# Kernel optimization log

Measured on AMD Instinct MI355X. Metric: run time of the kernel, lower is better.

## Reference

```python
import jax, jax.numpy as jnp
import numpy as np

NUM_VERTS = 6890
NUM_JOINTS = 24
NUM_BETAS = 10
NUM_POSE_FEATS = 207  # 23 joints * 9
NUM_COCO_JOINTS = 19
BATCH = 1024

SMPL_PARENTS = np.array([0, 0, 0, 0, 1, 2, 3, 4, 5, 6, 7, 8, 9, 9, 9,
                         12, 13, 14, 16, 17, 18, 19, 20, 21], dtype=np.int32)


def batch_rodrigues(theta):
    """theta: [N,3] axis-angle -> [N,3,3] rotation matrices (Rodrigues)."""
    angle = jnp.linalg.norm(theta + 1e-8, axis=1, keepdims=True)  # [N,1]
    r = theta / angle                                             # [N,3]
    c = jnp.cos(angle)[:, :, None]                                # [N,1,1]
    s = jnp.sin(angle)[:, :, None]
    rx, ry, rz = r[:, 0], r[:, 1], r[:, 2]
    zeros = jnp.zeros_like(rx)
    K = jnp.stack([zeros, -rz, ry,
                   rz, zeros, -rx,
                   -ry, rx, zeros], axis=1).reshape(-1, 3, 3)     # skew(r)
    eye = jnp.eye(3, dtype=theta.dtype)
    return eye + s * K + (1.0 - c) * jnp.matmul(K, K)


def batch_global_rigid_transformation(Rs, Js, parents, rotate_base=True):
    """Rs: [B,24,3,3], Js: [B,24,3]. Returns (new_J [B,24,3], A [B,24,4,4])."""
    B = Rs.shape[0]
    dtype = Rs.dtype
    if rotate_base:
        rot_x = jnp.array([[1., 0., 0.], [0., -1., 0.], [0., 0., -1.]], dtype=dtype)
        root_rot = jnp.matmul(Rs[:, 0], rot_x)
    else:
        root_rot = Rs[:, 0]

    bottom = jnp.broadcast_to(jnp.array([0., 0., 0., 1.], dtype=dtype), (B, 1, 4))

    def make_A(R, t):  # R [B,3,3], t [B,3] -> [B,4,4]
        top = jnp.concatenate([R, t[:, :, None]], axis=2)  # [B,3,4]
        return jnp.concatenate([top, bottom], axis=1)

    results = [make_A(root_rot, Js[:, 0])]
    for i in range(1, NUM_JOINTS):
        t_rel = Js[:, i] - Js[:, parents[i]]
        A_here = make_A(Rs[:, i], t_rel)
        results.append(jnp.matmul(results[parents[i]], A_here))
    results = jnp.stack(results, axis=1)  # [B,24,4,4]

    new_J = results[:, :, :3, 3]
    # A = results - pad(results @ [J;0]) : subtract rotated rest joint from translation
    t_adj = jnp.einsum('bjpq,bjq->bjp', results[:, :, :3, :3], Js)  # [B,24,3]
    A = results.at[:, :, :3, 3].add(-t_adj)
    return new_J, A


def setup_inputs() -> dict:
    key = jax.random.key(0)
    ks = jax.random.split(key, 8)
    beta = jax.random.normal(ks[0], (BATCH, NUM_BETAS), dtype=jnp.float32)
    theta = jax.random.normal(ks[1], (BATCH, NUM_JOINTS * 3), dtype=jnp.float32) * 0.3
    v_template = jax.random.normal(ks[2], (NUM_VERTS, 3), dtype=jnp.float32)
    shapedirs = jax.random.normal(ks[3], (NUM_BETAS, NUM_VERTS * 3), dtype=jnp.float32) * 0.01
    J_regressor = jax.random.uniform(ks[4], (NUM_JOINTS, NUM_VERTS), dtype=jnp.float32) / NUM_VERTS
    posedirs = jax.random.normal(ks[5], (NUM_POSE_FEATS, NUM_VERTS * 3), dtype=jnp.float32) * 0.01
    joint_regressor = jax.random.uniform(ks[6], (NUM_COCO_JOINTS, NUM_VERTS), dtype=jnp.float32) / NUM_VERTS
    w_raw = jax.random.uniform(ks[7], (NUM_VERTS, NUM_JOINTS), dtype=jnp.float32)
    weights = w_raw / jnp.sum(w_raw, axis=1, keepdims=True)  # LBS weights, rows sum to 1
    parents = jnp.asarray(SMPL_PARENTS)
    return {"beta": beta, "theta": theta, "v_template": v_template,
            "shapedirs": shapedirs, "J_regressor": J_regressor,
            "posedirs": posedirs, "joint_regressor": joint_regressor,
            "weights": weights, "parents": parents}


def reference(beta, theta, v_template, shapedirs, J_regressor,
              posedirs, joint_regressor, weights, parents):
    B = beta.shape[0]
    parents_np = np.asarray(parents)

    # Shape blendshapes: [B,10]@[10,20670] -> [B,6890,3]
    v_shaped = jnp.matmul(beta, shapedirs).reshape(B, NUM_VERTS, 3) + v_template

    J = jnp.einsum('bvd,jv->bjd', v_shaped, J_regressor)

    # Pose rotations
    Rs = batch_rodrigues(theta.reshape(-1, 3)).reshape(B, NUM_JOINTS, 3, 3)
    pose_feature = (Rs[:, 1:] - jnp.eye(3, dtype=Rs.dtype)).reshape(B, NUM_POSE_FEATS)
    v_posed = jnp.matmul(pose_feature, posedirs).reshape(B, NUM_VERTS, 3) + v_shaped

    # Kinematic chain
    J_transformed, A = batch_global_rigid_transformation(Rs, J, parents_np, rotate_base=True)

    # Linear blend skinning: per-vertex 4x4 transforms
    T = jnp.einsum('vj,bjpq->bvpq', weights, A)  # [B,6890,4,4]
    ones = jnp.ones((B, NUM_VERTS, 1), dtype=v_posed.dtype)
    v_posed_homo = jnp.concatenate([v_posed, ones], axis=2)  # [B,6890,4]
    verts = jnp.einsum('bvpq,bvq->bvp', T[:, :, :3, :], v_posed_homo)  # [B,6890,3]

    joints = jnp.einsum('bvd,jv->bjd', verts, joint_regressor)  # [B,19,3]
    return verts, joints, Rs
```

## Files before the change

### kernel.cpp

```cpp
#include <hip/hip_runtime.h>
#include <math.h>

#define NV   6890
#define NJ   24
#define NB   10
#define NPF  207
#define NCJ  19
#define BATCHN 1024
#define NC3  (NV*3)
#define KTOT 224
#define NVP  6892

#define OUT_JOINTS_OFF (BATCHN*NV*3)
#define OUT_RS_OFF     (OUT_JOINTS_OFF + BATCHN*NCJ*3)

#define WS_JS     0
#define WS_EF     1024
#define WS_AADJT  115712
#define WS_JRB    377856
#define WS_DIRST  443392
#define WS_END    2765824

typedef __attribute__((ext_vector_type(8))) short short8;
typedef __attribute__((ext_vector_type(4))) float f32x4;

__device__ __forceinline__ unsigned short f2bf(float f) {
    unsigned u = __float_as_uint(f);
    unsigned r = u + 0x7FFFu + ((u >> 16) & 1u);
    return (unsigned short)(r >> 16);
}
__device__ __forceinline__ float bf2f(unsigned short u) {
    return __uint_as_float((unsigned)u << 16);
}

__global__ __launch_bounds__(256) void smpl_kAP(
    const float* __restrict__ pdirs, const float* __restrict__ sdirs,
    unsigned short* __restrict__ dirsT,
    const float* __restrict__ jreg, const float* __restrict__ vtmpl,
    float* __restrict__ js,
    const float* __restrict__ jointreg, unsigned short* __restrict__ jrb) {
    int bx = blockIdx.x, t = threadIdx.x;
    if (bx < 216) {
        int vt = bx;
        for (int g = t; g < 2688; g += 256) {
            int frag = g >> 6, fo = g & 63;
            int ks = frag / 6, s = frag - ks * 6;
            int l15 = fo >> 2, lg = fo & 3;
            int gc = vt * 96 + s * 16 + l15;
            int k0 = ks * 32 + lg * 8;
            unsigned short pk[8];
#pragma unroll
            for (int i = 0; i < 8; i++) {
                int k = k0 + i;
                float val = 0.f;
                if (gc < NC3) {
                    if (k < NPF) val = pdirs[(size_t)k * NC3 + gc];
                    else if (k < NPF + NB) val = sdirs[(size_t)(k - NPF) * NC3 + gc];
                }
                pk[i] = f2bf(val);
            }
            *(short8*)(dirsT + (size_t)vt * 21504 + (size_t)g * 8) = *(const short8*)pk;
        }
        return;
    }
    if (bx >= 216 + NJ) {
        int j = bx - 216 - NJ;
        for (int v = t; v < NVP; v += 256)
            jrb[(size_t)j * NVP + v] = (v < NV) ? f2bf(jointreg[(size_t)j * NV + v]) : 0;
        return;
    }
    int j = bx - 216;
    float acc[33];
#pragma unroll
    for (int e = 0; e < 33; e++) acc[e] = 0.f;
    for (int v = t; v < NV; v += 256) {
        float w = jreg[j * NV + v];
#pragma unroll
        for (int k = 0; k < NB; k++) {
#pragma unroll
            for (int d = 0; d < 3; d++)
                acc[k * 3 + d] += w * sdirs[(size_t)k * NC3 + v * 3 + d];
        }
#pragma unroll
        for (int d = 0; d < 3; d++) acc[30 + d] += w * vtmpl[v * 3 + d];
    }
#pragma unroll
    for (int e = 0; e < 33; e++) {
#pragma unroll
        for (int off = 32; off >= 1; off >>= 1) acc[e] += __shfl_xor(acc[e], off, 64);
    }
    __shared__ float red[4][33];
    int lane = t & 63, wv = t >> 6;
    if (lane == 0) {
#pragma unroll
        for (int e = 0; e < 33; e++) red[wv][e] = acc[e];
    }
    __syncthreads();
    if (t < 33) js[j * 33 + t] = red[0][t] + red[1][t] + red[2][t] + red[3][t];
}

__global__ void smpl_kB(const float* __restrict__ theta, const float* __restrict__ beta_,
                        const float* __restrict__ js, float* __restrict__ outRs,
                        unsigned short* __restrict__ ef, unsigned short* __restrict__ aadjT,
                        float* __restrict__ outj) {
    int b = blockIdx.x;
    int t = threadIdx.x;
    __shared__ float Rl[NJ][9];
    __shared__ float Jl[NJ][3];
    __shared__ float Rw[NJ][12];

    if (t < 57) outj[(size_t)b * 57 + t] = 0.f;

    if (t < NJ) {
        int j = t;
        float tx = theta[b * 72 + j * 3 + 0];
        float ty = theta[b * 72 + j * 3 + 1];
        float tz = theta[b * 72 + j * 3 + 2];
        float ax = tx + 1e-8f, ay = ty + 1e-8f, az = tz + 1e-8f;
        float ang = sqrtf(ax * ax + ay * ay + az * az);
        float inv = 1.0f / ang;
        float rx = tx * inv, ry = ty * inv, rz = tz * inv;
        float s = sinf(ang), c = cosf(ang), t1 = 1.0f - c;
        float R[9];
        R[0] = 1.0f - t1 * (ry * ry + rz * rz);
        R[1] = -s * rz + t1 * rx * ry;
        R[2] =  s * ry + t1 * rx * rz;
        R[3] =  s * rz + t1 * rx * ry;
        R[4] = 1.0f - t1 * (rx * rx + rz * rz);
        R[5] = -s * rx + t1 * ry * rz;
        R[6] = -s * ry + t1 * rx * rz;
        R[7] =  s * rx + t1 * ry * rz;
        R[8] = 1.0f - t1 * (rx * rx + ry * ry);
#pragma unroll
        for (int e = 0; e < 9; e++) {
            Rl[j][e] = R[e];
            outRs[(size_t)b * 216 + j * 9 + e] = R[e];
        }
#pragma unroll
        for (int d = 0; d < 3; d++) {
            float accJ = js[j * 33 + 30 + d];
#pragma unroll
            for (int k = 0; k < NB; k++) accJ += beta_[b * NB + k] * js[j * 33 + k * 3 + d];
            Jl[j][d] = accJ;
        }
    }
    __syncthreads();
    for (int e = t; e < KTOT; e += 64) {
        float val;
        if (e < NPF) {
            int j = e / 9 + 1;
            int rc = e - (j - 1) * 9;
            val = Rl[j][rc] - ((rc == 0 || rc == 4 || rc == 8) ? 1.0f : 0.0f);
        } else if (e < NPF + NB) {
            val = beta_[b * NB + (e - NPF)];
        } else val = 0.f;
        ef[(size_t)b * KTOT + e] = f2bf(val);
    }
    if (t == 0) {
#pragma unroll
        for (int r = 0; r < 3; r++) {
            Rw[0][r * 4 + 0] =  Rl[0][r * 3 + 0];
            Rw[0][r * 4 + 1] = -Rl[0][r * 3 + 1];
            Rw[0][r * 4 + 2] = -Rl[0][r * 3 + 2];
            Rw[0][r * 4 + 3] =  Jl[0][r];
        }
        const int par[NJ] = {0,0,0,0,1,2,3,4,5,6,7,8,9,9,9,12,13,14,16,17,18,19,20,21};
#pragma unroll
        for (int i = 1; i < NJ; i++) {
            int p = par[i];
            float tr0 = Jl[i][0] - Jl[p][0];
            float tr1 = Jl[i][1] - Jl[p][1];
            float tr2 = Jl[i][2] - Jl[p][2];
#pragma unroll
            for (int r = 0; r < 3; r++) {
                float p0 = Rw[p][r * 4 + 0], p1 = Rw[p][r * 4 + 1], p2 = Rw[p][r * 4 + 2];
#pragma unroll
                for (int cc = 0; cc < 3; cc++)
                    Rw[i][r * 4 + cc] = p0 * Rl[i][0 + cc] + p1 * Rl[i][3 + cc] + p2 * Rl[i][6 + cc];
                Rw[i][r * 4 + 3] = p0 * tr0 + p1 * tr1 + p2 * tr2 + Rw[p][r * 4 + 3];
            }
        }
    }
    __syncthreads();
    for (int i = t; i < 512; i += 64) {
        int n = i >> 5, k = i & 31;
        float v = 0.f;
        if (n < 12 && k < 24) {
            int r = n >> 2, cc = n & 3;
            if (cc < 3) v = Rw[k][n];
            else v = Rw[k][r * 4 + 3] - (Rw[k][r * 4 + 0] * Jl[k][0] + Rw[k][r * 4 + 1] * Jl[k][1] +
                                         Rw[k][r * 4 + 2] * Jl[k][2]);
        }
        aadjT[(size_t)b * 512 + i] = f2bf(v);
    }
}

#define VPHI(v, bl, d) (((v) * 133 + (bl)) * 4 + (d))
__global__ __launch_bounds__(512, 4) void smpl_kC7(
    const unsigned short* __restrict__ dirsT, const float* __restrict__ vtmpl,
    const unsigned short* __restrict__ ef, const unsigned short* __restrict__ aadjT,
    const float* __restrict__ wts, float* __restrict__ outv) {
    __shared__ __align__(16) unsigned short dl[21504];
    __shared__ __align__(16) unsigned short vph[32 * 133 * 4];
    __shared__ unsigned short wbf[32][32];

    int tid = threadIdx.x;
    int vtile = blockIdx.x;
    int lane = tid & 63, wv = tid >> 6;
    int l15 = lane & 15, lg = lane >> 4;
    int fo = l15 * 4 + lg;

    {
        const uint2* src = (const uint2*)(dirsT + (size_t)vtile * 21504);
        uint2* dst = (uint2*)dl;
        for (int i = tid; i < 5376; i += 512) dst[i] = src[i];
    }
    for (int e = tid; e < 1024; e += 512) {
        int vl = e >> 5, k = e & 31;
        int gv = vtile * 32 + vl;
        float w = (k < NJ && gv < NV) ? wts[(size_t)gv * NJ + k] : 0.f;
        wbf[vl][k] = f2bf(w);
    }
    __syncthreads();

    short8 wf0 = *(const short8*)&wbf[l15][lg * 8];
    short8 wf1 = *(const short8*)&wbf[16 + l15][lg * 8];
    float vt[6];
#pragma unroll
    for (int s = 0; s < 6; s++) {
        int gcol = vtile * 96 + s * 16 + l15;
        vt[s] = (gcol < NC3) ? vtmpl[gcol] : 0.f;
    }

    for (int bt = 0; bt < 2; bt++) {
        int bb = (blockIdx.y * 2 + bt) * 128 + wv * 16;
        const short8* efr = (const short8*)(ef + (size_t)(bb + l15) * KTOT);
        short8 av[7];
#pragma unroll
        for (int ks = 0; ks < 7; ks++) av[ks] = efr[ks * 4 + lg];
        const short8* at0 = (const short8*)(aadjT + (size_t)bb * 512);
        short8 af0 = at0[fo];
        short8 af1 = at0[64 + fo];
        __builtin_amdgcn_sched_barrier(0);

        f32x4 acc[6];
#pragma unroll
        for (int s = 0; s < 6; s++) acc[s] = (f32x4){0.f, 0.f, 0.f, 0.f};
#pragma unroll
        for (int ks = 0; ks < 7; ks++) {
#pragma unroll
            for (int s = 0; s < 6; s++) {
                short8 bv = *(const short8*)&dl[((ks * 6 + s) << 9) + fo * 8];
                acc[s] = __builtin_amdgcn_mfma_f32_16x16x32_bf16(av[ks], bv, acc[s], 0, 0, 0);
            }
        }
#pragma unroll
        for (int s = 0; s < 6; s++) {
            int col = s * 16 + l15;
            int v = col / 3, d = col - v * 3;
            int bl0 = wv * 16 + lg * 4;
#pragma unroll
            for (int r = 0; r < 4; r++)
                vph[VPHI(v, bl0 + r, d)] = f2bf(acc[s][r] + vt[s]);
        }
#pragma unroll
        for (int bl2 = 0; bl2 < 16; bl2++) {
            short8 af = af0;
            af0 = af1;
            int nx = (bl2 + 2 < 16) ? (bl2 + 2) : 15;
            af1 = at0[nx * 64 + fo];
            f32x4 z = (f32x4){0.f, 0.f, 0.f, 0.f};
            f32x4 t0 = __builtin_amdgcn_mfma_f32_16x16x32_bf16(af, wf0, z, 0, 0, 0);
            f32x4 t1 = __builtin_amdgcn_mfma_f32_16x16x32_bf16(af, wf1, z, 0, 0, 0);
            int b = bb + bl2;
            int wvb = wv * 16 + bl2;
            if (lg < 3) {
                int p = lg;
                {
                    int vv = l15;
                    ushort4 xv = *(const ushort4*)&vph[VPHI(vv, wvb, 0)];
                    float o = fmaf(t0[0], bf2f(xv.x),
                              fmaf(t0[1], bf2f(xv.y), fmaf(t0[2], bf2f(xv.z), t0[3])));
                    int gv = vtile * 32 + vv;
                    if (gv < NV) outv[(size_t)b * NC3 + gv * 3 + p] = o;
                }
                {
                    int vv = 16 + l15;
                    ushort4 xv = *(const ushort4*)&vph[VPHI(vv, wvb, 0)];
                    float o = fmaf(t1[0], bf2f(xv.x),
                              fmaf(t1[1], bf2f(xv.y), fmaf(t1[2], bf2f(xv.z), t1[3])));
                    int gv = vtile * 32 + vv;
                    if (gv < NV) outv[(size_t)b * NC3 + gv * 3 + p] = o;
                }
            }
        }
    }
}

__global__ __launch_bounds__(256) void smpl_kD(
    const float* __restrict__ verts, const unsigned short* __restrict__ jrb,
    float* __restrict__ outj) {
    int tid = threadIdx.x;
    int b = blockIdx.x >> 1, half = blockIdx.x & 1;
    const float* vb = verts + (size_t)b * NC3;
    float acc[57];
#pragma unroll
    for (int e = 0; e < 57; e++) acc[e] = 0.f;

    int gend = half ? 1723 : 862;
    for (int it = 0; it < 4; it++) {
        int g = half * 862 + it * 256 + tid;
        if (g < gend) {
            int v = g * 4;
            const float* pa = vb + v * 3;
            float2 q0 = *(const float2*)(pa + 0);
            float2 q1 = *(const float2*)(pa + 2);
            float2 q2 = *(const float2*)(pa + 4);
            float2 q3 = *(const float2*)(pa + 6);
            float2 q4 = *(const float2*)(pa + 8);
            float2 q5 = *(const float2*)(pa + 10);
#pragma unroll
            for (int j = 0; j < NCJ; j++) {
                uint2 wp = *(const uint2*)(jrb + (size_t)j * NVP + v);
                float w0 = __uint_as_float((wp.x & 0xFFFFu) << 16);
                float w1 = __uint_as_float(wp.x & 0xFFFF0000u);
                float w2 = __uint_as_float((wp.y & 0xFFFFu) << 16);
                float w3 = __uint_as_float(wp.y & 0xFFFF0000u);
                acc[j * 3 + 0] += w0 * q0.x + w1 * q1.y + w2 * q3.x + w3 * q4.y;
                acc[j * 3 + 1] += w0 * q0.y + w1 * q2.x + w2 * q3.y + w3 * q5.x;
                acc[j * 3 + 2] += w0 * q1.x + w1 * q2.y + w2 * q4.x + w3 * q5.y;
            }
        }
    }
#pragma unroll
    for (int e = 0; e < 57; e++) {
#pragma unroll
        for (int off = 32; off >= 1; off >>= 1) acc[e] += __shfl_xor(acc[e], off, 64);
    }
    __shared__ float red[4][57];
    int lane = tid & 63, wv = tid >> 6;
    if (lane == 0) {
#pragma unroll
        for (int e = 0; e < 57; e++) red[wv][e] = acc[e];
    }
    __syncthreads();
    if (tid < 57)
        atomicAdd(&outj[(size_t)b * 57 + tid],
                  red[0][tid] + red[1][tid] + red[2][tid] + red[3][tid]);
}

extern "C" void kernel_launch(void* const* d_in, const int* in_sizes, int n_in,
                              void* d_out, int out_size, void* d_ws, size_t ws_size,
                              hipStream_t stream) {
    (void)in_sizes; (void)n_in; (void)out_size; (void)ws_size;
    const float* beta       = (const float*)d_in[0];
    const float* theta      = (const float*)d_in[1];
    const float* v_template = (const float*)d_in[2];
    const float* shapedirs  = (const float*)d_in[3];
    const float* jreg       = (const float*)d_in[4];
    const float* posedirs   = (const float*)d_in[5];
    const float* jointreg   = (const float*)d_in[6];
    const float* weights    = (const float*)d_in[7];
    float* out = (float*)d_out;
    float* ws  = (float*)d_ws;
    unsigned short* ef    = (unsigned short*)(ws + WS_EF);
    unsigned short* aadjT = (unsigned short*)(ws + WS_AADJT);
    unsigned short* jrb   = (unsigned short*)(ws + WS_JRB);
    unsigned short* dirsT = (unsigned short*)(ws + WS_DIRST);

    smpl_kAP<<<216 + NJ + NCJ, 256, 0, stream>>>(posedirs, shapedirs, dirsT,
                                                 jreg, v_template, ws + WS_JS,
                                                 jointreg, jrb);
    smpl_kB<<<BATCHN, 64, 0, stream>>>(theta, beta, ws + WS_JS, out + OUT_RS_OFF,
                                       ef, aadjT, out + OUT_JOINTS_OFF);
    dim3 gC(216, 4);
    smpl_kC7<<<gC, 512, 0, stream>>>(dirsT, v_template, ef, aadjT, weights, out);
    smpl_kD<<<2 * BATCHN, 256, 0, stream>>>(out, jrb, out + OUT_JOINTS_OFF);
}
```

Before: 127.6 us.

## Batch-prefetch skinning transforms in chunks and process four batch tiles per block

In the skinning kernel, each block now loops over four 128-sample batch tiles instead of two, and the grid's y dimension is halved. This amortises the per-block staging of directions and weights into shared memory over more work. The per-sample transform loads are restructured from a rolling two-deep prefetch into two chunks of eight register-held loads, with the first chunk issued during the blendshape MFMA phase. Empty asm barriers pin the loads in place. The costs are higher register pressure and only 432 blocks, which may reduce occupancy and load balance.

```diff
diff --git a/kernel.cpp b/kernel.cpp
--- a/kernel.cpp
+++ b/kernel.cpp
@@ -232,16 +232,14 @@
         vt[s] = (gcol < NC3) ? vtmpl[gcol] : 0.f;
     }
 
-    for (int bt = 0; bt < 2; bt++) {
-        int bb = (blockIdx.y * 2 + bt) * 128 + wv * 16;
+    for (int bt = 0; bt < 4; bt++) {
+        int bb = (blockIdx.y * 4 + bt) * 128 + wv * 16;
         const short8* efr = (const short8*)(ef + (size_t)(bb + l15) * KTOT);
         short8 av[7];
 #pragma unroll
         for (int ks = 0; ks < 7; ks++) av[ks] = efr[ks * 4 + lg];
-        const short8* at0 = (const short8*)(aadjT + (size_t)bb * 512);
-        short8 af0 = at0[fo];
-        short8 af1 = at0[64 + fo];
-        __builtin_amdgcn_sched_barrier(0);
+#pragma unroll
+        for (int ks = 0; ks < 7; ks++) asm volatile("" : "+v"(av[ks]));
 
         f32x4 acc[6];
 #pragma unroll
@@ -254,6 +252,11 @@
                 acc[s] = __builtin_amdgcn_mfma_f32_16x16x32_bf16(av[ks], bv, acc[s], 0, 0, 0);
             }
         }
+        const short8* at0 = (const short8*)(aadjT + (size_t)bb * 512);
+        short8 afc[8];
+#pragma unroll
+        for (int i = 0; i < 8; i++) afc[i] = at0[i * 64 + fo];
+
 #pragma unroll
         for (int s = 0; s < 6; s++) {
             int col = s * 16 + l15;
@@ -264,33 +267,46 @@
                 vph[VPHI(v, bl0 + r, d)] = f2bf(acc[s][r] + vt[s]);
         }
 #pragma unroll
-        for (int bl2 = 0; bl2 < 16; bl2++) {
-            short8 af = af0;
-            af0 = af1;
-            int nx = (bl2 + 2 < 16) ? (bl2 + 2) : 15;
-            af1 = at0[nx * 64 + fo];
-            f32x4 z = (f32x4){0.f, 0.f, 0.f, 0.f};
-            f32x4 t0 = __builtin_amdgcn_mfma_f32_16x16x32_bf16(af, wf0, z, 0, 0, 0);
-            f32x4 t1 = __builtin_amdgcn_mfma_f32_16x16x32_bf16(af, wf1, z, 0, 0, 0);
-            int b = bb + bl2;
-            int wvb = wv * 16 + bl2;
-            if (lg < 3) {
-                int p = lg;
-                {
-                    int vv = l15;
-                    ushort4 xv = *(const ushort4*)&vph[VPHI(vv, wvb, 0)];
-                    float o = fmaf(t0[0], bf2f(xv.x),
-                              fmaf(t0[1], bf2f(xv.y), fmaf(t0[2], bf2f(xv.z), t0[3])));
-                    int gv = vtile * 32 + vv;
-                    if (gv < NV) outv[(size_t)b * NC3 + gv * 3 + p] = o;
-                }
-                {
-                    int vv = 16 + l15;
-                    ushort4 xv = *(const ushort4*)&vph[VPHI(vv, wvb, 0)];
-                    float o = fmaf(t1[0], bf2f(xv.x),
-                              fmaf(t1[1], bf2f(xv.y), fmaf(t1[2], bf2f(xv.z), t1[3])));
-                    int gv = vtile * 32 + vv;
-                    if (gv < NV) outv[(size_t)b * NC3 + gv * 3 + p] = o;
+        for (int i = 0; i < 8; i++) asm volatile("" : "+v"(afc[i]));
+        short8 afn[8];
+#pragma unroll
+        for (int i = 0; i < 8; i++) afn[i] = at0[(8 + i) * 64 + fo];
+
+#pragma unroll
+        for (int ch = 0; ch < 2; ch++) {
+            if (ch == 1) {
+#pragma unroll
+                for (int i = 0; i < 8; i++) asm volatile("" : "+v"(afn[i]));
+#pragma unroll
+                for (int i = 0; i < 8; i++) afc[i] = afn[i];
+            }
+#pragma unroll
+            for (int i = 0; i < 8; i++) {
+                short8 af = afc[i];
+                f32x4 z = (f32x4){0.f, 0.f, 0.f, 0.f};
+                f32x4 t0 = __builtin_amdgcn_mfma_f32_16x16x32_bf16(af, wf0, z, 0, 0, 0);
+                f32x4 t1 = __builtin_amdgcn_mfma_f32_16x16x32_bf16(af, wf1, z, 0, 0, 0);
+                int bl2 = ch * 8 + i;
+                int b = bb + bl2;
+                int wvb = wv * 16 + bl2;
+                if (lg < 3) {
+                    int p = lg;
+                    {
+                        int vv = l15;
+                        ushort4 xv = *(const ushort4*)&vph[VPHI(vv, wvb, 0)];
+                        float o = fmaf(t0[0], bf2f(xv.x),
+                                  fmaf(t0[1], bf2f(xv.y), fmaf(t0[2], bf2f(xv.z), t0[3])));
+                        int gv = vtile * 32 + vv;
+                        if (gv < NV) outv[(size_t)b * NC3 + gv * 3 + p] = o;
+                    }
+                    {
+                        int vv = 16 + l15;
+                        ushort4 xv = *(const ushort4*)&vph[VPHI(vv, wvb, 0)];
+                        float o = fmaf(t1[0], bf2f(xv.x),
+                                  fmaf(t1[1], bf2f(xv.y), fmaf(t1[2], bf2f(xv.z), t1[3])));
+                        int gv = vtile * 32 + vv;
+                        if (gv < NV) outv[(size_t)b * NC3 + gv * 3 + p] = o;
+                    }
                 }
             }
         }
@@ -373,7 +389,7 @@
                                                  jointreg, jrb);
     smpl_kB<<<BATCHN, 64, 0, stream>>>(theta, beta, ws + WS_JS, out + OUT_RS_OFF,
                                        ef, aadjT, out + OUT_JOINTS_OFF);
-    dim3 gC(216, 4);
+    dim3 gC(216, 2);
     smpl_kC7<<<gC, 512, 0, stream>>>(dirsT, v_template, ef, aadjT, weights, out);
     smpl_kD<<<2 * BATCHN, 256, 0, stream>>>(out, jrb, out + OUT_JOINTS_OFF);
 }
```

Measured after the change: 127.3 us. Within noise of the previous version (-0.2%).

## Drop LDS staging of blend-shape dirs in skinning kernel, use smaller blocks

Applied to the files above, without the earlier changes.

The skinning kernel no longer stages the 43KB bf16 direction tile in shared memory. Each wave now reads its B fragments straight from global memory, and blocks shrink to 256 threads covering 64 batch rows on a 216x16 grid. This cuts LDS use so more blocks can be resident per CU, at the cost of the same dirs tile being re-read from global/L2 by every block. The prep kernel's dirs-transpose stage is also split across six times as many blocks to expose more parallelism.

```diff
diff --git a/kernel.cpp b/kernel.cpp
--- a/kernel.cpp
+++ b/kernel.cpp
@@ -40,9 +40,9 @@
     float* __restrict__ js,
     const float* __restrict__ jointreg, unsigned short* __restrict__ jrb) {
     int bx = blockIdx.x, t = threadIdx.x;
-    if (bx < 216) {
-        int vt = bx;
-        for (int g = t; g < 2688; g += 256) {
+    if (bx < 216 * 6) {
+        int vt = bx / 6, part = bx - (bx / 6) * 6;
+        for (int g = part * 448 + t; g < part * 448 + 448; g += 256) {
             int frag = g >> 6, fo = g & 63;
             int ks = frag / 6, s = frag - ks * 6;
             int l15 = fo >> 2, lg = fo & 3;
@@ -63,13 +63,13 @@
         }
         return;
     }
-    if (bx >= 216 + NJ) {
-        int j = bx - 216 - NJ;
+    if (bx >= 216 * 6 + NJ) {
+        int j = bx - 216 * 6 - NJ;
         for (int v = t; v < NVP; v += 256)
             jrb[(size_t)j * NVP + v] = (v < NV) ? f2bf(jointreg[(size_t)j * NV + v]) : 0;
         return;
     }
-    int j = bx - 216;
+    int j = bx - 216 * 6;
     float acc[33];
 #pragma unroll
     for (int e = 0; e < 33; e++) acc[e] = 0.f;
@@ -195,27 +195,22 @@
     }
 }
 
-#define VPHI(v, bl, d) (((v) * 133 + (bl)) * 4 + (d))
-__global__ __launch_bounds__(512, 4) void smpl_kC7(
+#define VPHI(v, bl, d) (((v) * 66 + (bl)) * 4 + (d))
+__global__ __launch_bounds__(256, 8) void smpl_kC8(
     const unsigned short* __restrict__ dirsT, const float* __restrict__ vtmpl,
     const unsigned short* __restrict__ ef, const unsigned short* __restrict__ aadjT,
     const float* __restrict__ wts, float* __restrict__ outv) {
-    __shared__ __align__(16) unsigned short dl[21504];
-    __shared__ __align__(16) unsigned short vph[32 * 133 * 4];
+    __shared__ __align__(16) unsigned short vph[32 * 66 * 4];
     __shared__ unsigned short wbf[32][32];
 
     int tid = threadIdx.x;
     int vtile = blockIdx.x;
+    int btile = blockIdx.y * 64;
     int lane = tid & 63, wv = tid >> 6;
     int l15 = lane & 15, lg = lane >> 4;
     int fo = l15 * 4 + lg;
 
-    {
-        const uint2* src = (const uint2*)(dirsT + (size_t)vtile * 21504);
-        uint2* dst = (uint2*)dl;
-        for (int i = tid; i < 5376; i += 512) dst[i] = src[i];
-    }
-    for (int e = tid; e < 1024; e += 512) {
+    for (int e = tid; e < 1024; e += 256) {
         int vl = e >> 5, k = e & 31;
         int gv = vtile * 32 + vl;
         float w = (k < NJ && gv < NV) ? wts[(size_t)gv * NJ + k] : 0.f;
@@ -232,66 +227,62 @@
         vt[s] = (gcol < NC3) ? vtmpl[gcol] : 0.f;
     }
 
-    for (int bt = 0; bt < 2; bt++) {
-        int bb = (blockIdx.y * 2 + bt) * 128 + wv * 16;
-        const short8* efr = (const short8*)(ef + (size_t)(bb + l15) * KTOT);
-        short8 av[7];
-#pragma unroll
-        for (int ks = 0; ks < 7; ks++) av[ks] = efr[ks * 4 + lg];
-        const short8* at0 = (const short8*)(aadjT + (size_t)bb * 512);
-        short8 af0 = at0[fo];
-        short8 af1 = at0[64 + fo];
-        __builtin_amdgcn_sched_barrier(0);
-
-        f32x4 acc[6];
-#pragma unroll
-        for (int s = 0; s < 6; s++) acc[s] = (f32x4){0.f, 0.f, 0.f, 0.f};
-#pragma unroll
-        for (int ks = 0; ks < 7; ks++) {
-#pragma unroll
-            for (int s = 0; s < 6; s++) {
-                short8 bv = *(const short8*)&dl[((ks * 6 + s) << 9) + fo * 8];
-                acc[s] = __builtin_amdgcn_mfma_f32_16x16x32_bf16(av[ks], bv, acc[s], 0, 0, 0);
-            }
-        }
+    const short8* efr = (const short8*)(ef + (size_t)(btile + wv * 16 + l15) * KTOT);
+    const short8* bfr = (const short8*)(dirsT + (size_t)vtile * 21504);
+    short8 av[7];
+#pragma unroll
+    for (int ks = 0; ks < 7; ks++) av[ks] = efr[ks * 4 + lg];
+    f32x4 acc[6];
+#pragma unroll
+    for (int s = 0; s < 6; s++) acc[s] = (f32x4){0.f, 0.f, 0.f, 0.f};
+#pragma unroll
+    for (int ks = 0; ks < 7; ks++) {
 #pragma unroll
         for (int s = 0; s < 6; s++) {
-            int col = s * 16 + l15;
-            int v = col / 3, d = col - v * 3;
-            int bl0 = wv * 16 + lg * 4;
-#pragma unroll
-            for (int r = 0; r < 4; r++)
-                vph[VPHI(v, bl0 + r, d)] = f2bf(acc[s][r] + vt[s]);
-        }
-#pragma unroll
-        for (int bl2 = 0; bl2 < 16; bl2++) {
-            short8 af = af0;
-            af0 = af1;
-            int nx = (bl2 + 2 < 16) ? (bl2 + 2) : 15;
-            af1 = at0[nx * 64 + fo];
-            f32x4 z = (f32x4){0.f, 0.f, 0.f, 0.f};
-            f32x4 t0 = __builtin_amdgcn_mfma_f32_16x16x32_bf16(af, wf0, z, 0, 0, 0);
-            f32x4 t1 = __builtin_amdgcn_mfma_f32_16x16x32_bf16(af, wf1, z, 0, 0, 0);
-            int b = bb + bl2;
-            int wvb = wv * 16 + bl2;
-            if (lg < 3) {
-                int p = lg;
-                {
-                    int vv = l15;
-                    ushort4 xv = *(const ushort4*)&vph[VPHI(vv, wvb, 0)];
-                    float o = fmaf(t0[0], bf2f(xv.x),
-                              fmaf(t0[1], bf2f(xv.y), fmaf(t0[2], bf2f(xv.z), t0[3])));
-                    int gv = vtile * 32 + vv;
-                    if (gv < NV) outv[(size_t)b * NC3 + gv * 3 + p] = o;
-                }
-                {
-                    int vv = 16 + l15;
-                    ushort4 xv = *(const ushort4*)&vph[VPHI(vv, wvb, 0)];
-                    float o = fmaf(t1[0], bf2f(xv.x),
-                              fmaf(t1[1], bf2f(xv.y), fmaf(t1[2], bf2f(xv.z), t1[3])));
-                    int gv = vtile * 32 + vv;
-                    if (gv < NV) outv[(size_t)b * NC3 + gv * 3 + p] = o;
-                }
+            short8 bv = bfr[(ks * 6 + s) * 64 + fo];
+            acc[s] = __builtin_amdgcn_mfma_f32_16x16x32_bf16(av[ks], bv, acc[s], 0, 0, 0);
+        }
+    }
+#pragma unroll
+    for (int s = 0; s < 6; s++) {
+        int col = s * 16 + l15;
+        int v = col / 3, d = col - v * 3;
+        int bl0 = wv * 16 + lg * 4;
+#pragma unroll
+        for (int r = 0; r < 4; r++)
+            vph[VPHI(v, bl0 + r, d)] = f2bf(acc[s][r] + vt[s]);
+    }
+    const short8* at0 = (const short8*)(aadjT + (size_t)(btile + wv * 16) * 512);
+    short8 af0 = at0[fo];
+    short8 af1 = at0[64 + fo];
+#pragma unroll
+    for (int bl2 = 0; bl2 < 16; bl2++) {
+        short8 af = af0;
+        af0 = af1;
+        int nx = (bl2 + 2 < 16) ? (bl2 + 2) : 15;
+        af1 = at0[nx * 64 + fo];
+        f32x4 z = (f32x4){0.f, 0.f, 0.f, 0.f};
+        f32x4 t0 = __builtin_amdgcn_mfma_f32_16x16x32_bf16(af, wf0, z, 0, 0, 0);
+        f32x4 t1 = __builtin_amdgcn_mfma_f32_16x16x32_bf16(af, wf1, z, 0, 0, 0);
+        int b = btile + wv * 16 + bl2;
+        int wvb = wv * 16 + bl2;
+        if (lg < 3) {
+            int p = lg;
+            {
+                int vv = l15;
+                ushort4 xv = *(const ushort4*)&vph[VPHI(vv, wvb, 0)];
+                float o = fmaf(t0[0], bf2f(xv.x),
+                          fmaf(t0[1], bf2f(xv.y), fmaf(t0[2], bf2f(xv.z), t0[3])));
+                int gv = vtile * 32 + vv;
+                if (gv < NV) outv[(size_t)b * NC3 + gv * 3 + p] = o;
+            }
+            {
+                int vv = 16 + l15;
+                ushort4 xv = *(const ushort4*)&vph[VPHI(vv, wvb, 0)];
+                float o = fmaf(t1[0], bf2f(xv.x),
+                          fmaf(t1[1], bf2f(xv.y), fmaf(t1[2], bf2f(xv.z), t1[3])));
+                int gv = vtile * 32 + vv;
+                if (gv < NV) outv[(size_t)b * NC3 + gv * 3 + p] = o;
             }
         }
     }
@@ -368,12 +359,12 @@
     unsigned short* jrb   = (unsigned short*)(ws + WS_JRB);
     unsigned short* dirsT = (unsigned short*)(ws + WS_DIRST);
 
-    smpl_kAP<<<216 + NJ + NCJ, 256, 0, stream>>>(posedirs, shapedirs, dirsT,
-                                                 jreg, v_template, ws + WS_JS,
-                                                 jointreg, jrb);
+    smpl_kAP<<<216 * 6 + NJ + NCJ, 256, 0, stream>>>(posedirs, shapedirs, dirsT,
+                                                     jreg, v_template, ws + WS_JS,
+                                                     jointreg, jrb);
     smpl_kB<<<BATCHN, 64, 0, stream>>>(theta, beta, ws + WS_JS, out + OUT_RS_OFF,
                                        ef, aadjT, out + OUT_JOINTS_OFF);
-    dim3 gC(216, 4);
-    smpl_kC7<<<gC, 512, 0, stream>>>(dirsT, v_template, ef, aadjT, weights, out);
+    dim3 gC(216, 16);
+    smpl_kC8<<<gC, 256, 0, stream>>>(dirsT, v_template, ef, aadjT, weights, out);
     smpl_kD<<<2 * BATCHN, 256, 0, stream>>>(out, jrb, out + OUT_JOINTS_OFF);
 }
```

After: 149.6 us. 1.17x slower.
